# Kernel tuning notes

Measured on AMD Instinct MI355X. Metric: run time of the kernel, lower is better.

The kernel has to match this reference:

```python
import jax, jax.numpy as jnp
import numpy as np

N, E = 10000, 160000
DIN, H, DOUT, DE = 128, 256, 256, 32


def _lin(k, din, dout, scale=0.05):
    return jax.random.normal(k, (din, dout), jnp.float32) * scale


def setup_inputs() -> dict:
    key = jax.random.key(0)
    ks = jax.random.split(key, 40)
    inp = {}
    inp["x"] = jax.random.normal(ks[0], (N, DIN), jnp.float32)
    inp["edge_attr"] = jax.random.normal(ks[1], (E, DE), jnp.float32)
    inp["src"] = jax.random.randint(ks[2], (E,), 0, N, jnp.int32)
    inp["dst"] = jax.random.randint(ks[3], (E,), 0, N, jnp.int32)
    # encoders
    inp["W_edge_enc"] = _lin(ks[4], DE, H); inp["b_edge_enc"] = jnp.zeros((H,), jnp.float32)
    inp["W_node_enc"] = _lin(ks[5], DIN, H); inp["b_node_enc"] = jnp.zeros((H,), jnp.float32)
    # 3 TransformerConv layers (heads=1): q,k,v (with bias), edge (no bias), skip (with bias)
    outs = [H, H, DOUT]
    i = 6
    for l, C in enumerate(outs, start=1):
        inp[f"Wq{l}"] = _lin(ks[i], H, C); i += 1
        inp[f"bq{l}"] = jnp.zeros((C,), jnp.float32)
        inp[f"Wk{l}"] = _lin(ks[i], H, C); i += 1
        inp[f"bk{l}"] = jnp.zeros((C,), jnp.float32)
        inp[f"Wv{l}"] = _lin(ks[i], H, C); i += 1
        inp[f"bv{l}"] = jnp.zeros((C,), jnp.float32)
        inp[f"We{l}"] = _lin(ks[i], H, C); i += 1
        inp[f"Ws{l}"] = _lin(ks[i], H, C); i += 1
        inp[f"bs{l}"] = jnp.zeros((C,), jnp.float32)
    return inp


def _tconv(x, src, dst, edge_emb, Wq, bq, Wk, bk, Wv, bv, We, Ws, bs):
    # PyG TransformerConv, heads=1, concat=True, root_weight=True
    n = x.shape[0]
    C = Wq.shape[1]
    q = x @ Wq + bq            # [N, C]
    k = x @ Wk + bk            # [N, C]
    v = x @ Wv + bv            # [N, C]
    e = edge_emb @ We          # [E, C] (lin_edge, no bias)
    kj = k[src] + e            # [E, C]
    alpha = jnp.sum(q[dst] * kj, axis=-1) / jnp.sqrt(jnp.float32(C))  # [E]
    # segment softmax over incoming edges per target node
    m = jax.ops.segment_max(alpha, dst, num_segments=n)
    a = jnp.exp(alpha - m[dst])
    denom = jax.ops.segment_sum(a, dst, num_segments=n)
    a = a / jnp.maximum(denom[dst], 1e-16)
    msg = (v[src] + e) * a[:, None]                       # [E, C]
    out = jax.ops.segment_sum(msg, dst, num_segments=n)   # [N, C]
    return out + x @ Ws + bs                               # root skip


def reference(x, edge_attr, src, dst,
              W_edge_enc, b_edge_enc, W_node_enc, b_node_enc,
              Wq1, bq1, Wk1, bk1, Wv1, bv1, We1, Ws1, bs1,
              Wq2, bq2, Wk2, bk2, Wv2, bv2, We2, Ws2, bs2,
              Wq3, bq3, Wk3, bk3, Wv3, bv3, We3, Ws3, bs3):
    relu = jax.nn.relu
    edge_feat = relu(edge_attr @ W_edge_enc + b_edge_enc)  # [E, H]
    h = relu(x @ W_node_enc + b_node_enc)                  # [N, H]
    # dropout(0.3) is identity in eval mode
    h = relu(_tconv(h, src, dst, edge_feat, Wq1, bq1, Wk1, bk1, Wv1, bv1, We1, Ws1, bs1))
    h = relu(_tconv(h, src, dst, edge_feat, Wq2, bq2, Wk2, bk2, Wv2, bv2, We2, Ws2, bs2))
    h = _tconv(h, src, dst, edge_feat, Wq3, bq3, Wk3, bk3, Wv3, bv3, We3, Ws3, bs3)
    return h
```

## Files before the change

### kernel.cpp

```cpp
#include <hip/hip_runtime.h>
#include <cstdint>

typedef unsigned short u16;
typedef __attribute__((ext_vector_type(8))) short short8;
typedef __attribute__((ext_vector_type(8))) __bf16 bf16x8;
typedef __attribute__((ext_vector_type(4))) float f32x4;

#define DEV __device__ __forceinline__

DEV u16 f2bf(float f){
  uint32_t u = __float_as_uint(f);
  u += 0x7fffu + ((u >> 16) & 1u);
  return (u16)(u >> 16);
}
DEV float bf2f(u16 h){ return __uint_as_float(((uint32_t)h) << 16); }

DEV f32x4 mfma16(short8 a, short8 b, f32x4 c){
  return __builtin_amdgcn_mfma_f32_16x16x32_bf16(
      __builtin_bit_cast(bf16x8, a), __builtin_bit_cast(bf16x8, b), c, 0, 0, 0);
}

#define NN 10000
#define EE 160000
#define MPN 10112
#define MPE 160128

__global__ void count_k(const int* __restrict__ dst, int* __restrict__ cnt){
  int i = blockIdx.x * 256 + threadIdx.x;
  if(i < EE) atomicAdd(&cnt[dst[i]], 1);
}

__global__ void scan1_k(const int* __restrict__ cnt, int* __restrict__ offs,
                        int* __restrict__ bsum){
  __shared__ int buf[256];
  int b = blockIdx.x, tid = threadIdx.x, i = b * 256 + tid;
  int v = (i < NN) ? cnt[i] : 0;
  buf[tid] = v; __syncthreads();
  for(int d = 1; d < 256; d <<= 1){
    int t = (tid >= d) ? buf[tid - d] : 0;
    __syncthreads();
    buf[tid] += t;
    __syncthreads();
  }
  if(i < NN) offs[i] = buf[tid] - v;
  if(tid == 255) bsum[b] = buf[255];
}

__global__ void scan23_k(int* __restrict__ offs, const int* __restrict__ bsum,
                         int* __restrict__ cursor){
  __shared__ int bpre_s;
  int b = blockIdx.x, tid = threadIdx.x;
  if(tid == 0){
    int s = 0;
    for(int i = 0; i < b; ++i) s += bsum[i];
    bpre_s = s;
  }
  __syncthreads();
  int i = b * 256 + tid;
  if(i < NN){ int v = offs[i] + bpre_s; offs[i] = v; cursor[i] = v; }
  if(i == 0) offs[NN] = EE;
}

__global__ void scatter_k(const int* __restrict__ dst, int* __restrict__ cursor,
                          int* __restrict__ eids){
  int i = blockIdx.x * 256 + threadIdx.x;
  if(i < EE){ int p = atomicAdd(&cursor[dst[i]], 1); eids[p] = i; }
}

__global__ void rank_k(const int* __restrict__ dst, const int* __restrict__ src,
                       const int* __restrict__ offs, const int* __restrict__ eids,
                       int* __restrict__ eidp, int* __restrict__ srcp){
  int e = blockIdx.x * 256 + threadIdx.x;
  if(e >= MPE) return;
  if(e >= EE){ eidp[e] = e; return; }
  int n = dst[e];
  int p0 = offs[n], p1 = offs[n + 1];
  int rk = 0;
  for(int p = p0; p < p1; ++p) rk += (eids[p] < e) ? 1 : 0;
  int slot = p0 + rk;
  eidp[slot] = e;
  srcp[slot] = src[e];
}

struct WPack {
  const float* Wq[3]; const float* Wk[3]; const float* Wv[3];
  const float* Ws[3]; const float* We[3];
  const float* bq[3]; const float* bk[3]; const float* bv[3]; const float* bs[3];
};

#define PG0 5056
#define PG1 (PG0 + 20016)
#define PG2 (PG1 + 3840)
#define PG3 (PG2 + 1536)
#define PG4 (PG3 + 15)
#define PG5 (PG4 + 256)

__global__ __launch_bounds__(256) void prep_all_k(
    const float* __restrict__ x, const float* __restrict__ eattr, WPack P,
    const float* __restrict__ Wne, const float* __restrict__ Wee,
    u16* __restrict__ xbf, u16* __restrict__ eabf,
    u16* __restrict__ Wcat, u16* __restrict__ Wet,
    u16* __restrict__ WqBF, u16* __restrict__ WeBF,
    float* __restrict__ biasc, u16* __restrict__ Wnet, u16* __restrict__ Weet)
{
  int b = blockIdx.x, tid = threadIdx.x;
  if(b < PG0){
    int i = b * 256 + tid;
    xbf[i] = (i < NN * 128) ? f2bf(x[i]) : (u16)0;
  } else if(b < PG1){
    int i = (b - PG0) * 256 + tid;
    eabf[i] = (i < EE * 32) ? f2bf(eattr[i]) : (u16)0;
  } else if(b < PG2){
    int b2 = b - PG1; int l = b2 / 1280, r = b2 % 1280; int k = tid;
    float v;
    if(r < 256)       v = P.Wq[l][k * 256 + r];
    else if(r < 512)  v = P.Ws[l][k * 256 + (r - 256)];
    else if(r < 768){ Wet[((size_t)l * 256 + (r - 512)) * 256 + k] =
                        f2bf(P.We[l][k * 256 + (r - 512)]); return; }
    else if(r < 1024) v = P.Wk[l][k * 256 + (r - 768)];
    else              v = P.Wv[l][k * 256 + (r - 1024)];
    Wcat[((size_t)l * 1280 + r) * 256 + k] = f2bf(v);
  } else if(b < PG3){
    int b3 = b - PG2; int l = b3 >> 9, rr = b3 & 511; int t = tid;
    if(rr < 256) WqBF[((size_t)l * 256 + rr) * 256 + t] = f2bf(P.Wq[l][rr * 256 + t]);
    else         WeBF[((size_t)l * 256 + (rr - 256)) * 256 + t] = f2bf(P.We[l][(rr - 256) * 256 + t]);
  } else if(b < PG4){
    int b4 = b - PG3; int l = b4 / 5, seg = b4 % 5; int t = tid;
    float v;
    if(seg == 0)      v = P.bq[l][t];
    else if(seg == 1) v = P.bs[l][t];
    else if(seg == 2){
      const float* we = P.We[l] + (size_t)t * 256; const float* bq = P.bq[l];
      float s = 0.f;
      for(int c = 0; c < 256; ++c) s += bq[c] * we[c];
      v = s;
    }
    else if(seg == 3) v = P.bk[l][t];
    else              v = P.bv[l][t];
    biasc[(size_t)l * 1280 + seg * 256 + t] = v;
  } else {
    int n = b - PG4;
    if(tid < 128) Wnet[n * 128 + tid] = f2bf(Wne[(size_t)tid * 256 + n]);
    if(tid < 32)  Weet[n * 32 + tid]  = f2bf(Wee[(size_t)tid * 256 + n]);
  }
}

template<int BK, int EPI, int AG = 0>
__global__ __launch_bounds__(256) void gemm_k(
    const u16* __restrict__ A, const u16* __restrict__ Bt,
    const float* __restrict__ bias, void* __restrict__ Out,
    const float* __restrict__ accv, const float* __restrict__ skipS,
    const int* __restrict__ rowmap, u16* __restrict__ kvout,
    int Mreal, int Nld, int K, size_t sA, size_t sB, size_t sOb)
{
  constexpr int CPR = BK / 8;
  constexpr int SW  = (BK == 64) ? 7 : 3;
  __shared__ short8 smem8[2048];
  u16* Al = (u16*)smem8;
  u16* Bl = Al + 128 * BK;
  A  += (size_t)blockIdx.z * sA;
  Bt += (size_t)blockIdx.z * sB;
  Out = (void*)((char*)Out + (size_t)blockIdx.z * sOb);
  int tid = threadIdx.x, lane = tid & 63;
  int rowBase = blockIdx.x * 128, colBase = blockIdx.y * 128;
  int wave = tid >> 6, wm = wave >> 1, wn = wave & 1;
  int lr = lane & 15, lk = lane >> 4;
  f32x4 acc[4][4] = {};
  int nkt = K / BK;
  for(int kt = 0; kt < nkt; ++kt){
    __syncthreads();
    for(int ci = tid; ci < 128 * CPR; ci += 256){
      int r = ci / CPR, cb = ci % CPR;
      int ar = AG ? rowmap[rowBase + r] : (rowBase + r);
      int d = (r * CPR + (cb ^ (r & SW))) * 8;
      *(short8*)&Al[d] = *(const short8*)&A [(size_t)ar * K + kt * BK + cb * 8];
      *(short8*)&Bl[d] = *(const short8*)&Bt[(size_t)(colBase + r) * K + kt * BK + cb * 8];
    }
    __syncthreads();
    #pragma unroll
    for(int kk = 0; kk < BK / 32; ++kk){
      short8 af[4], bfr[4];
      #pragma unroll
      for(int m = 0; m < 4; ++m){
        int r = wm * 64 + m * 16 + lr;
        int byt = r * (BK * 2) + kk * 64 + lk * 16; byt ^= (r & SW) << 4;
        af[m] = *(const short8*)((const char*)Al + byt);
      }
      #pragma unroll
      for(int n = 0; n < 4; ++n){
        int r = wn * 64 + n * 16 + lr;
        int byt = r * (BK * 2) + kk * 64 + lk * 16; byt ^= (r & SW) << 4;
        bfr[n] = *(const short8*)((const char*)Bl + byt);
      }
      #pragma unroll
      for(int m = 0; m < 4; ++m)
        #pragma unroll
        for(int n = 0; n < 4; ++n)
          acc[m][n] = mfma16(af[m], bfr[n], acc[m][n]);
    }
  }

  __syncthreads();
  if constexpr(EPI == 0 || EPI == 4){
    bool kvside = (EPI == 0) && (colBase >= 768);
    if(kvside){
      u16* us = (u16*)smem8;
      #pragma unroll
      for(int m = 0; m < 4; ++m)
        #pragma unroll
        for(int n = 0; n < 4; ++n){
          int cc = wn * 64 + n * 16 + lr;
          #pragma unroll
          for(int j = 0; j < 4; ++j){
            int rr = wm * 64 + m * 16 + lk * 4 + j;
            us[rr * 128 + cc] = f2bf(acc[m][n][j] + bias[colBase + cc]);
          }
        }
      __syncthreads();
      for(int ch = tid; ch < 2048; ch += 256){
        int rr = ch >> 4, cc = (ch & 15) << 3;
        int r = rowBase + rr;
        if(r < Mreal)
          *(short8*)&kvout[(size_t)r * 512 + (colBase - 768) + cc] = *(short8*)&us[rr * 128 + cc];
      }
    } else {
      float* fs = (float*)smem8;
      #pragma unroll
      for(int h = 0; h < 2; ++h){
        if(wm == h){
          #pragma unroll
          for(int m = 0; m < 4; ++m)
            #pragma unroll
            for(int n = 0; n < 4; ++n){
              int cc = wn * 64 + n * 16 + lr;
              int c = colBase + cc;
              #pragma unroll
              for(int j = 0; j < 4; ++j){
                int r2 = m * 16 + lk * 4 + j;
                float v = acc[m][n][j];
                if constexpr(EPI == 0) v += bias[c];
                else {
                  int r = rowBase + h * 64 + r2;
                  v += accv[(size_t)r * 256 + c] + skipS[(size_t)r * 768 + 256 + c];
                }
                fs[r2 * 128 + cc] = v;
              }
            }
        }
        __syncthreads();
        for(int ch = tid; ch < 2048; ch += 256){
          int rr = ch >> 5, cc = (ch & 31) << 2;
          int r = rowBase + h * 64 + rr;
          if(r < Mreal)
            *(float4*)&((float*)Out)[(size_t)r * Nld + colBase + cc] = *(float4*)&fs[rr * 128 + cc];
        }
        __syncthreads();
      }
    }
  } else {
    u16* us = (u16*)smem8;
    #pragma unroll
    for(int m = 0; m < 4; ++m)
      #pragma unroll
      for(int n = 0; n < 4; ++n){
        int cc = wn * 64 + n * 16 + lr;
        int c = colBase + cc;
        #pragma unroll
        for(int j = 0; j < 4; ++j){
          int rr = wm * 64 + m * 16 + lk * 4 + j;
          float v = acc[m][n][j];
          if constexpr(EPI == 1){ v += bias[c]; v = fmaxf(v, 0.f); }
          else if constexpr(EPI == 3){
            int r = rowBase + rr;
            v += accv[(size_t)r * 256 + c] + skipS[(size_t)r * 768 + 256 + c];
            v = fmaxf(v, 0.f);
          }
          us[rr * 128 + cc] = f2bf(v);
        }
      }
    __syncthreads();
    for(int ch = tid; ch < 2048; ch += 256){
      int rr = ch >> 4, cc = (ch & 15) << 3;
      int r = rowBase + rr;
      if(r < Mreal)
        *(short8*)&((u16*)Out)[(size_t)r * Nld + colBase + cc] = *(short8*)&us[rr * 128 + cc];
    }
  }
}

__global__ __launch_bounds__(256) void node_pass_k(
    const float* __restrict__ slab, const u16* __restrict__ efp,
    const u16* __restrict__ kvbf,
    const int* __restrict__ srcp, const int* __restrict__ offs,
    float* __restrict__ accv, u16* __restrict__ aggef)
{
  int wave = threadIdx.x >> 6, lane = threadIdx.x & 63;
  int n = blockIdx.x * 4 + wave;
  if(n >= NN) return;
  int li = lane & 15, eg = lane >> 4;
  const float* qrow = slab + (size_t)n * 768 + li * 16;
  float q[16], e[16];
  #pragma unroll
  for(int t = 0; t < 4; ++t){
    float4 a = *(const float4*)(qrow + t * 4);
    float4 b = *(const float4*)(qrow + 512 + t * 4);
    q[t*4+0] = a.x; q[t*4+1] = a.y; q[t*4+2] = a.z; q[t*4+3] = a.w;
    e[t*4+0] = b.x; e[t*4+1] = b.y; e[t*4+2] = b.z; e[t*4+3] = b.w;
  }
  float av[16], ag[16];
  #pragma unroll
  for(int d = 0; d < 16; ++d){ av[d] = 0.f; ag[d] = 0.f; }
  float den = 0.f;
  int p0 = offs[n], pe = offs[n + 1];
  int p = p0 + eg;
  for(; p + 4 < pe; p += 8){
    int s1 = srcp[p], s2 = srcp[p + 4];
    const u16* kv1 = kvbf + ((size_t)s1 << 9) + li * 16;
    const u16* kv2 = kvbf + ((size_t)s2 << 9) + li * 16;
    const u16* ef1 = efp + ((size_t)p << 8) + li * 16;
    const u16* ef2 = efp + ((size_t)(p + 4) << 8) + li * 16;
    short8 kA1 = *(const short8*)(kv1),       kB1 = *(const short8*)(kv1 + 8);
    short8 vA1 = *(const short8*)(kv1 + 256), vB1 = *(const short8*)(kv1 + 264);
    short8 fA1 = *(const short8*)(ef1),       fB1 = *(const short8*)(ef1 + 8);
    short8 kA2 = *(const short8*)(kv2),       kB2 = *(const short8*)(kv2 + 8);
    short8 vA2 = *(const short8*)(kv2 + 256), vB2 = *(const short8*)(kv2 + 264);
    short8 fA2 = *(const short8*)(ef2),       fB2 = *(const short8*)(ef2 + 8);
    float sc1 = 0.f, sc2 = 0.f;
    #pragma unroll
    for(int d = 0; d < 8; ++d){
      sc1 += q[d]   * bf2f((u16)kA1[d]) + e[d]   * bf2f((u16)fA1[d]);
      sc1 += q[8+d] * bf2f((u16)kB1[d]) + e[8+d] * bf2f((u16)fB1[d]);
      sc2 += q[d]   * bf2f((u16)kA2[d]) + e[d]   * bf2f((u16)fA2[d]);
      sc2 += q[8+d] * bf2f((u16)kB2[d]) + e[8+d] * bf2f((u16)fB2[d]);
    }
    sc1 += __shfl_xor(sc1, 1); sc2 += __shfl_xor(sc2, 1);
    sc1 += __shfl_xor(sc1, 2); sc2 += __shfl_xor(sc2, 2);
    sc1 += __shfl_xor(sc1, 4); sc2 += __shfl_xor(sc2, 4);
    sc1 += __shfl_xor(sc1, 8); sc2 += __shfl_xor(sc2, 8);
    float w1 = __expf(sc1 * 0.0625f);
    float w2 = __expf(sc2 * 0.0625f);
    den += w1 + w2;
    #pragma unroll
    for(int d = 0; d < 8; ++d){
      av[d]   += w1 * bf2f((u16)vA1[d]) + w2 * bf2f((u16)vA2[d]);
      av[8+d] += w1 * bf2f((u16)vB1[d]) + w2 * bf2f((u16)vB2[d]);
      ag[d]   += w1 * bf2f((u16)fA1[d]) + w2 * bf2f((u16)fA2[d]);
      ag[8+d] += w1 * bf2f((u16)fB1[d]) + w2 * bf2f((u16)fB2[d]);
    }
  }
  if(p < pe){
    int s = srcp[p];
    const u16* kvp = kvbf + ((size_t)s << 9) + li * 16;
    const u16* epp = efp + ((size_t)p << 8) + li * 16;
    short8 kA = *(const short8*)(kvp);
    short8 kB = *(const short8*)(kvp + 8);
    short8 vA = *(const short8*)(kvp + 256);
    short8 vB = *(const short8*)(kvp + 264);
    short8 fA = *(const short8*)(epp);
    short8 fB = *(const short8*)(epp + 8);
    float part = 0.f;
    #pragma unroll
    for(int d = 0; d < 8; ++d){
      part += q[d]   * bf2f((u16)kA[d]) + e[d]   * bf2f((u16)fA[d]);
      part += q[8+d] * bf2f((u16)kB[d]) + e[8+d] * bf2f((u16)fB[d]);
    }
    part += __shfl_xor(part, 1);
    part += __shfl_xor(part, 2);
    part += __shfl_xor(part, 4);
    part += __shfl_xor(part, 8);
    float wgt = __expf(part * 0.0625f);
    den += wgt;
    #pragma unroll
    for(int d = 0; d < 8; ++d){
      av[d]   += wgt * bf2f((u16)vA[d]);
      av[8+d] += wgt * bf2f((u16)vB[d]);
      ag[d]   += wgt * bf2f((u16)fA[d]);
      ag[8+d] += wgt * bf2f((u16)fB[d]);
    }
  }
  #pragma unroll
  for(int d = 0; d < 16; ++d){
    av[d] += __shfl_xor(av[d], 16); av[d] += __shfl_xor(av[d], 32);
    ag[d] += __shfl_xor(ag[d], 16); ag[d] += __shfl_xor(ag[d], 32);
  }
  den += __shfl_xor(den, 16); den += __shfl_xor(den, 32);
  float rden = 1.f / fmaxf(den, 1e-16f);
  if(eg == 0){
    float* ao = accv + (size_t)n * 256 + li * 16;
    #pragma unroll
    for(int t = 0; t < 4; ++t){
      float4 o;
      o.x = av[t*4+0] * rden; o.y = av[t*4+1] * rden;
      o.z = av[t*4+2] * rden; o.w = av[t*4+3] * rden;
      *(float4*)(ao + t * 4) = o;
    }
  } else if(eg == 1){
    u16* go = aggef + (size_t)n * 256 + li * 16;
    #pragma unroll
    for(int t = 0; t < 2; ++t){
      short8 o;
      #pragma unroll
      for(int d = 0; d < 8; ++d) o[d] = (short)f2bf(ag[t*8+d] * rden);
      *(short8*)(go + t * 8) = o;
    }
  }
}

extern "C" void kernel_launch(void* const* d_in, const int* in_sizes, int n_in,
                              void* d_out, int out_size, void* d_ws, size_t ws_size,
                              hipStream_t stream){
  const float* x     = (const float*)d_in[0];
  const float* eattr = (const float*)d_in[1];
  const int*   src   = (const int*)d_in[2];
  const int*   dst   = (const int*)d_in[3];
  const float* Wee   = (const float*)d_in[4];
  const float* bee   = (const float*)d_in[5];
  const float* Wne   = (const float*)d_in[6];
  const float* bne   = (const float*)d_in[7];
  WPack P;
  for(int l = 0; l < 3; ++l){
    const int b = 8 + l * 9;
    P.Wq[l] = (const float*)d_in[b + 0]; P.bq[l] = (const float*)d_in[b + 1];
    P.Wk[l] = (const float*)d_in[b + 2]; P.bk[l] = (const float*)d_in[b + 3];
    P.Wv[l] = (const float*)d_in[b + 4]; P.bv[l] = (const float*)d_in[b + 5];
    P.We[l] = (const float*)d_in[b + 6];
    P.Ws[l] = (const float*)d_in[b + 7]; P.bs[l] = (const float*)d_in[b + 8];
  }

  char* w = (char*)d_ws; size_t off = 0;
  auto alloc = [&](size_t bytes)->char*{
    char* p = w + off; off = (off + bytes + 255) & ~(size_t)255; return p;
  };
  u16*   Wcat  = (u16*)  alloc((size_t)3 * 1280 * 256 * 2);
  u16*   Wet   = (u16*)  alloc((size_t)3 * 256 * 256 * 2);
  u16*   WqBF  = (u16*)  alloc((size_t)3 * 256 * 256 * 2);
  u16*   WeBF  = (u16*)  alloc((size_t)3 * 256 * 256 * 2);
  float* biasc = (float*)alloc((size_t)3 * 1280 * 4);
  u16*   Wnet  = (u16*)  alloc((size_t)256 * 128 * 2);
  u16*   Weet  = (u16*)  alloc((size_t)256 * 32 * 2);
  u16*   xbf   = (u16*)  alloc((size_t)MPN * 128 * 2);
  u16*   eabf  = (u16*)  alloc((size_t)MPE * 32 * 2);
  u16*   hbf   = (u16*)  alloc((size_t)MPN * 256 * 2);
  float* slab  = (float*)alloc((size_t)MPN * 768 * 4);
  u16*   kvbf  = (u16*)  alloc((size_t)MPN * 512 * 2);
  u16*   efp   = (u16*)  alloc((size_t)MPE * 256 * 2);
  int*   cnt   = (int*)  alloc((size_t)NN * 4);
  int*   offs  = (int*)  alloc((size_t)(NN + 1) * 4);
  int*   cursor= (int*)  alloc((size_t)NN * 4);
  int*   bsum  = (int*)  alloc((size_t)64 * 4);
  int*   eids  = (int*)  alloc((size_t)EE * 4);
  int*   eidp  = (int*)  alloc((size_t)MPE * 4);
  int*   srcp  = (int*)  alloc((size_t)EE * 4);
  float* accv  = (float*)alloc((size_t)MPN * 256 * 4);
  u16*   aggef = (u16*)  alloc((size_t)MPN * 256 * 2);
  if(off > ws_size) return;

  hipMemsetAsync(cnt, 0, (size_t)NN * 4, stream);
  count_k <<<(EE + 255) / 256, 256, 0, stream>>>(dst, cnt);
  scan1_k <<<40, 256, 0, stream>>>(cnt, offs, bsum);
  scan23_k<<<40, 256, 0, stream>>>(offs, bsum, cursor);
  scatter_k<<<(EE + 255) / 256, 256, 0, stream>>>(dst, cursor, eids);
  rank_k  <<<(MPE + 255) / 256, 256, 0, stream>>>(dst, src, offs, eids, eidp, srcp);

  prep_all_k<<<PG5, 256, 0, stream>>>(x, eattr, P, Wne, Wee,
      xbf, eabf, Wcat, Wet, WqBF, WeBF, biasc, Wnet, Weet);

  gemm_k<64,5><<<dim3(2, 2, 3), 256, 0, stream>>>(
      WeBF, WqBF, nullptr, Wcat + (size_t)512 * 256,
      nullptr, nullptr, nullptr, nullptr, 256, 256, 256,
      (size_t)256 * 256, (size_t)256 * 256, (size_t)1280 * 256 * 2);

  gemm_k<64,1><<<dim3(MPN / 128, 2), 256, 0, stream>>>(
      xbf, Wnet, bne, hbf, nullptr, nullptr, nullptr, nullptr, NN, 256, 128, 0, 0, 0);
  gemm_k<32,1,1><<<dim3(MPE / 128, 2), 256, 0, stream>>>(
      eabf, Weet, bee, efp, nullptr, nullptr, eidp, nullptr, EE, 256, 32, 0, 0, 0);

  for(int l = 0; l < 3; ++l){
    gemm_k<64,0><<<dim3(MPN / 128, 10), 256, 0, stream>>>(
        hbf, Wcat + (size_t)l * 1280 * 256, biasc + (size_t)l * 1280, slab,
        nullptr, nullptr, nullptr, kvbf, NN, 768, 256, 0, 0, 0);
    node_pass_k<<<NN / 4, 256, 0, stream>>>(slab, efp, kvbf, srcp, offs, accv, aggef);
    if(l < 2)
      gemm_k<64,3><<<dim3(MPN / 128, 2), 256, 0, stream>>>(
          aggef, Wet + (size_t)l * 256 * 256, nullptr, hbf,
          accv, slab, nullptr, nullptr, NN, 256, 256, 0, 0, 0);
    else
      gemm_k<64,4><<<dim3(MPN / 128, 2), 256, 0, stream>>>(
          aggef, Wet + (size_t)l * 256 * 256, nullptr, d_out,
          accv, slab, nullptr, nullptr, NN, 256, 256, 0, 0, 0);
  }
}
```

Baseline: 353.1 us.

## Store q/qe projections as bf16 and map one node per 16-lane group

The fused projection GEMM epilogue now writes the q and q·We sections as bf16 into a separate buffer, and the skip section as fp32 into its own compact 256-wide buffer, replacing the 768-wide fp32 slab. The node pass assigns one node to each 16-lane group instead of one per wave. Lanes load source indices cooperatively and broadcast them with shuffles, which removes the cross-group reductions. This cuts memory traffic for the slab and aims to keep lanes busy on low-degree nodes, at the cost of bf16 rounding of q and longer serial edge loops per group.

```diff
diff --git a/kernel.cpp b/kernel.cpp
--- a/kernel.cpp
+++ b/kernel.cpp
@@ -151,6 +151,7 @@
     const float* __restrict__ bias, void* __restrict__ Out,
     const float* __restrict__ accv, const float* __restrict__ skipS,
     const int* __restrict__ rowmap, u16* __restrict__ kvout,
+    float* __restrict__ skipOut,
     int Mreal, int Nld, int K, size_t sA, size_t sB, size_t sOb)
 {
   constexpr int CPR = BK / 8;
@@ -201,9 +202,35 @@
   }
 
   __syncthreads();
-  if constexpr(EPI == 0 || EPI == 4){
-    bool kvside = (EPI == 0) && (colBase >= 768);
-    if(kvside){
+  if constexpr(EPI == 0){
+    int sec = colBase >> 8;
+    if(sec == 1){
+      float* fs = (float*)smem8;
+      #pragma unroll
+      for(int h = 0; h < 2; ++h){
+        if(wm == h){
+          #pragma unroll
+          for(int m = 0; m < 4; ++m)
+            #pragma unroll
+            for(int n = 0; n < 4; ++n){
+              int cc = wn * 64 + n * 16 + lr;
+              #pragma unroll
+              for(int j = 0; j < 4; ++j){
+                int r2 = m * 16 + lk * 4 + j;
+                fs[r2 * 128 + cc] = acc[m][n][j] + bias[colBase + cc];
+              }
+            }
+        }
+        __syncthreads();
+        for(int ch = tid; ch < 2048; ch += 256){
+          int rr = ch >> 5, cc = (ch & 31) << 2;
+          int r = rowBase + h * 64 + rr;
+          if(r < Mreal)
+            *(float4*)&skipOut[(size_t)r * 256 + (colBase - 256) + cc] = *(float4*)&fs[rr * 128 + cc];
+        }
+        __syncthreads();
+      }
+    } else {
       u16* us = (u16*)smem8;
       #pragma unroll
       for(int m = 0; m < 4; ++m)
@@ -217,45 +244,45 @@
           }
         }
       __syncthreads();
+      u16* dstp; int cofs;
+      if(sec == 0){ dstp = (u16*)Out; cofs = colBase; }
+      else if(sec == 2){ dstp = (u16*)Out; cofs = colBase - 256; }
+      else { dstp = kvout; cofs = colBase - 768; }
       for(int ch = tid; ch < 2048; ch += 256){
         int rr = ch >> 4, cc = (ch & 15) << 3;
         int r = rowBase + rr;
         if(r < Mreal)
-          *(short8*)&kvout[(size_t)r * 512 + (colBase - 768) + cc] = *(short8*)&us[rr * 128 + cc];
-      }
-    } else {
-      float* fs = (float*)smem8;
-      #pragma unroll
-      for(int h = 0; h < 2; ++h){
-        if(wm == h){
+          *(short8*)&dstp[(size_t)r * 512 + cofs + cc] = *(short8*)&us[rr * 128 + cc];
+      }
+    }
+  } else if constexpr(EPI == 4){
+    float* fs = (float*)smem8;
+    #pragma unroll
+    for(int h = 0; h < 2; ++h){
+      if(wm == h){
+        #pragma unroll
+        for(int m = 0; m < 4; ++m)
           #pragma unroll
-          for(int m = 0; m < 4; ++m)
+          for(int n = 0; n < 4; ++n){
+            int cc = wn * 64 + n * 16 + lr;
+            int c = colBase + cc;
             #pragma unroll
-            for(int n = 0; n < 4; ++n){
-              int cc = wn * 64 + n * 16 + lr;
-              int c = colBase + cc;
-              #pragma unroll
-              for(int j = 0; j < 4; ++j){
-                int r2 = m * 16 + lk * 4 + j;
-                float v = acc[m][n][j];
-                if constexpr(EPI == 0) v += bias[c];
-                else {
-                  int r = rowBase + h * 64 + r2;
-                  v += accv[(size_t)r * 256 + c] + skipS[(size_t)r * 768 + 256 + c];
-                }
-                fs[r2 * 128 + cc] = v;
-              }
+            for(int j = 0; j < 4; ++j){
+              int r2 = m * 16 + lk * 4 + j;
+              int r = rowBase + h * 64 + r2;
+              fs[r2 * 128 + cc] = acc[m][n][j]
+                + accv[(size_t)r * 256 + c] + skipS[(size_t)r * 256 + c];
             }
-        }
-        __syncthreads();
-        for(int ch = tid; ch < 2048; ch += 256){
-          int rr = ch >> 5, cc = (ch & 31) << 2;
-          int r = rowBase + h * 64 + rr;
-          if(r < Mreal)
-            *(float4*)&((float*)Out)[(size_t)r * Nld + colBase + cc] = *(float4*)&fs[rr * 128 + cc];
-        }
-        __syncthreads();
-      }
+          }
+      }
+      __syncthreads();
+      for(int ch = tid; ch < 2048; ch += 256){
+        int rr = ch >> 5, cc = (ch & 31) << 2;
+        int r = rowBase + h * 64 + rr;
+        if(r < Mreal)
+          *(float4*)&((float*)Out)[(size_t)r * Nld + colBase + cc] = *(float4*)&fs[rr * 128 + cc];
+      }
+      __syncthreads();
     }
   } else {
     u16* us = (u16*)smem8;
@@ -272,7 +299,7 @@
           if constexpr(EPI == 1){ v += bias[c]; v = fmaxf(v, 0.f); }
           else if constexpr(EPI == 3){
             int r = rowBase + rr;
-            v += accv[(size_t)r * 256 + c] + skipS[(size_t)r * 768 + 256 + c];
+            v += accv[(size_t)r * 256 + c] + skipS[(size_t)r * 256 + c];
             v = fmaxf(v, 0.f);
           }
           us[rr * 128 + cc] = f2bf(v);
@@ -289,120 +316,115 @@
 }
 
 __global__ __launch_bounds__(256) void node_pass_k(
-    const float* __restrict__ slab, const u16* __restrict__ efp,
+    const u16* __restrict__ qq, const u16* __restrict__ efp,
     const u16* __restrict__ kvbf,
     const int* __restrict__ srcp, const int* __restrict__ offs,
     float* __restrict__ accv, u16* __restrict__ aggef)
 {
-  int wave = threadIdx.x >> 6, lane = threadIdx.x & 63;
-  int n = blockIdx.x * 4 + wave;
+  int tid = threadIdx.x, lane = tid & 63;
+  int li = lane & 15, gb = lane & 48;
+  int n = blockIdx.x * 16 + (tid >> 4);
   if(n >= NN) return;
-  int li = lane & 15, eg = lane >> 4;
-  const float* qrow = slab + (size_t)n * 768 + li * 16;
+  const u16* qrow = qq + (size_t)n * 512 + li * 16;
+  short8 qh0 = *(const short8*)(qrow),       qh1 = *(const short8*)(qrow + 8);
+  short8 eh0 = *(const short8*)(qrow + 256), eh1 = *(const short8*)(qrow + 264);
   float q[16], e[16];
   #pragma unroll
-  for(int t = 0; t < 4; ++t){
-    float4 a = *(const float4*)(qrow + t * 4);
-    float4 b = *(const float4*)(qrow + 512 + t * 4);
-    q[t*4+0] = a.x; q[t*4+1] = a.y; q[t*4+2] = a.z; q[t*4+3] = a.w;
-    e[t*4+0] = b.x; e[t*4+1] = b.y; e[t*4+2] = b.z; e[t*4+3] = b.w;
+  for(int d = 0; d < 8; ++d){
+    q[d] = bf2f((u16)qh0[d]); q[8 + d] = bf2f((u16)qh1[d]);
+    e[d] = bf2f((u16)eh0[d]); e[8 + d] = bf2f((u16)eh1[d]);
   }
   float av[16], ag[16];
   #pragma unroll
   for(int d = 0; d < 16; ++d){ av[d] = 0.f; ag[d] = 0.f; }
   float den = 0.f;
-  int p0 = offs[n], pe = offs[n + 1];
-  int p = p0 + eg;
-  for(; p + 4 < pe; p += 8){
-    int s1 = srcp[p], s2 = srcp[p + 4];
-    const u16* kv1 = kvbf + ((size_t)s1 << 9) + li * 16;
-    const u16* kv2 = kvbf + ((size_t)s2 << 9) + li * 16;
-    const u16* ef1 = efp + ((size_t)p << 8) + li * 16;
-    const u16* ef2 = efp + ((size_t)(p + 4) << 8) + li * 16;
-    short8 kA1 = *(const short8*)(kv1),       kB1 = *(const short8*)(kv1 + 8);
-    short8 vA1 = *(const short8*)(kv1 + 256), vB1 = *(const short8*)(kv1 + 264);
-    short8 fA1 = *(const short8*)(ef1),       fB1 = *(const short8*)(ef1 + 8);
-    short8 kA2 = *(const short8*)(kv2),       kB2 = *(const short8*)(kv2 + 8);
-    short8 vA2 = *(const short8*)(kv2 + 256), vB2 = *(const short8*)(kv2 + 264);
-    short8 fA2 = *(const short8*)(ef2),       fB2 = *(const short8*)(ef2 + 8);
-    float sc1 = 0.f, sc2 = 0.f;
+  int p0 = offs[n], deg = offs[n + 1] - p0;
+  for(int base = 0; base < deg; base += 16){
+    int scnt = deg - base; if(scnt > 16) scnt = 16;
+    int ssrc = (li < scnt) ? srcp[p0 + base + li] : 0;
+    int jj = 0;
+    for(; jj + 1 < scnt; jj += 2){
+      int s1 = __shfl(ssrc, gb + jj);
+      int s2 = __shfl(ssrc, gb + jj + 1);
+      size_t p1 = (size_t)(p0 + base + jj);
+      const u16* kv1 = kvbf + ((size_t)s1 << 9) + li * 16;
+      const u16* kv2 = kvbf + ((size_t)s2 << 9) + li * 16;
+      const u16* e1 = efp + (p1 << 8) + li * 16;
+      const u16* e2 = efp + ((p1 + 1) << 8) + li * 16;
+      short8 kA1 = *(const short8*)(kv1),       kB1 = *(const short8*)(kv1 + 8);
+      short8 vA1 = *(const short8*)(kv1 + 256), vB1 = *(const short8*)(kv1 + 264);
+      short8 fA1 = *(const short8*)(e1),        fB1 = *(const short8*)(e1 + 8);
+      short8 kA2 = *(const short8*)(kv2),       kB2 = *(const short8*)(kv2 + 8);
+      short8 vA2 = *(const short8*)(kv2 + 256), vB2 = *(const short8*)(kv2 + 264);
+      short8 fA2 = *(const short8*)(e2),        fB2 = *(const short8*)(e2 + 8);
+      float sc1 = 0.f, sc2 = 0.f;
+      #pragma unroll
+      for(int d = 0; d < 8; ++d){
+        sc1 += q[d]   * bf2f((u16)kA1[d]) + e[d]   * bf2f((u16)fA1[d]);
+        sc1 += q[8+d] * bf2f((u16)kB1[d]) + e[8+d] * bf2f((u16)fB1[d]);
+        sc2 += q[d]   * bf2f((u16)kA2[d]) + e[d]   * bf2f((u16)fA2[d]);
+        sc2 += q[8+d] * bf2f((u16)kB2[d]) + e[8+d] * bf2f((u16)fB2[d]);
+      }
+      sc1 += __shfl_xor(sc1, 1); sc2 += __shfl_xor(sc2, 1);
+      sc1 += __shfl_xor(sc1, 2); sc2 += __shfl_xor(sc2, 2);
+      sc1 += __shfl_xor(sc1, 4); sc2 += __shfl_xor(sc2, 4);
+      sc1 += __shfl_xor(sc1, 8); sc2 += __shfl_xor(sc2, 8);
+      float w1 = __expf(sc1 * 0.0625f);
+      float w2 = __expf(sc2 * 0.0625f);
+      den += w1 + w2;
+      #pragma unroll
+      for(int d = 0; d < 8; ++d){
+        av[d]   += w1 * bf2f((u16)vA1[d]) + w2 * bf2f((u16)vA2[d]);
+        av[8+d] += w1 * bf2f((u16)vB1[d]) + w2 * bf2f((u16)vB2[d]);
+        ag[d]   += w1 * bf2f((u16)fA1[d]) + w2 * bf2f((u16)fA2[d]);
+        ag[8+d] += w1 * bf2f((u16)fB1[d]) + w2 * bf2f((u16)fB2[d]);
+      }
+    }
+    if(jj < scnt){
+      int s = __shfl(ssrc, gb + jj);
+      size_t p = (size_t)(p0 + base + jj);
+      const u16* kvp = kvbf + ((size_t)s << 9) + li * 16;
+      const u16* ep = efp + (p << 8) + li * 16;
+      short8 kA = *(const short8*)(kvp),       kB = *(const short8*)(kvp + 8);
+      short8 vA = *(const short8*)(kvp + 256), vB = *(const short8*)(kvp + 264);
+      short8 fA = *(const short8*)(ep),        fB = *(const short8*)(ep + 8);
+      float part = 0.f;
+      #pragma unroll
+      for(int d = 0; d < 8; ++d){
+        part += q[d]   * bf2f((u16)kA[d]) + e[d]   * bf2f((u16)fA[d]);
+        part += q[8+d] * bf2f((u16)kB[d]) + e[8+d] * bf2f((u16)fB[d]);
+      }
+      part += __shfl_xor(part, 1);
+      part += __shfl_xor(part, 2);
+      part += __shfl_xor(part, 4);
+      part += __shfl_xor(part, 8);
+      float wgt = __expf(part * 0.0625f);
+      den += wgt;
+      #pragma unroll
+      for(int d = 0; d < 8; ++d){
+        av[d]   += wgt * bf2f((u16)vA[d]);
+        av[8+d] += wgt * bf2f((u16)vB[d]);
+        ag[d]   += wgt * bf2f((u16)fA[d]);
+        ag[8+d] += wgt * bf2f((u16)fB[d]);
+      }
+    }
+  }
+  float rden = 1.f / fmaxf(den, 1e-16f);
+  float* ao = accv + (size_t)n * 256 + li * 16;
+  #pragma unroll
+  for(int t = 0; t < 4; ++t){
+    float4 o;
+    o.x = av[t*4+0] * rden; o.y = av[t*4+1] * rden;
+    o.z = av[t*4+2] * rden; o.w = av[t*4+3] * rden;
+    *(float4*)(ao + t * 4) = o;
+  }
+  u16* go = aggef + (size_t)n * 256 + li * 16;
+  #pragma unroll
+  for(int t = 0; t < 2; ++t){
+    short8 o;
     #pragma unroll
-    for(int d = 0; d < 8; ++d){
-      sc1 += q[d]   * bf2f((u16)kA1[d]) + e[d]   * bf2f((u16)fA1[d]);
-      sc1 += q[8+d] * bf2f((u16)kB1[d]) + e[8+d] * bf2f((u16)fB1[d]);
-      sc2 += q[d]   * bf2f((u16)kA2[d]) + e[d]   * bf2f((u16)fA2[d]);
-      sc2 += q[8+d] * bf2f((u16)kB2[d]) + e[8+d] * bf2f((u16)fB2[d]);
-    }
-    sc1 += __shfl_xor(sc1, 1); sc2 += __shfl_xor(sc2, 1);
-    sc1 += __shfl_xor(sc1, 2); sc2 += __shfl_xor(sc2, 2);
-    sc1 += __shfl_xor(sc1, 4); sc2 += __shfl_xor(sc2, 4);
-    sc1 += __shfl_xor(sc1, 8); sc2 += __shfl_xor(sc2, 8);
-    float w1 = __expf(sc1 * 0.0625f);
-    float w2 = __expf(sc2 * 0.0625f);
-    den += w1 + w2;
-    #pragma unroll
-    for(int d = 0; d < 8; ++d){
-      av[d]   += w1 * bf2f((u16)vA1[d]) + w2 * bf2f((u16)vA2[d]);
-      av[8+d] += w1 * bf2f((u16)vB1[d]) + w2 * bf2f((u16)vB2[d]);
-      ag[d]   += w1 * bf2f((u16)fA1[d]) + w2 * bf2f((u16)fA2[d]);
-      ag[8+d] += w1 * bf2f((u16)fB1[d]) + w2 * bf2f((u16)fB2[d]);
-    }
-  }
-  if(p < pe){
-    int s = srcp[p];
-    const u16* kvp = kvbf + ((size_t)s << 9) + li * 16;
-    const u16* epp = efp + ((size_t)p << 8) + li * 16;
-    short8 kA = *(const short8*)(kvp);
-    short8 kB = *(const short8*)(kvp + 8);
-    short8 vA = *(const short8*)(kvp + 256);
-    short8 vB = *(const short8*)(kvp + 264);
-    short8 fA = *(const short8*)(epp);
-    short8 fB = *(const short8*)(epp + 8);
-    float part = 0.f;
-    #pragma unroll
-    for(int d = 0; d < 8; ++d){
-      part += q[d]   * bf2f((u16)kA[d]) + e[d]   * bf2f((u16)fA[d]);
-      part += q[8+d] * bf2f((u16)kB[d]) + e[8+d] * bf2f((u16)fB[d]);
-    }
-    part += __shfl_xor(part, 1);
-    part += __shfl_xor(part, 2);
-    part += __shfl_xor(part, 4);
-    part += __shfl_xor(part, 8);
-    float wgt = __expf(part * 0.0625f);
-    den += wgt;
-    #pragma unroll
-    for(int d = 0; d < 8; ++d){
-      av[d]   += wgt * bf2f((u16)vA[d]);
-      av[8+d] += wgt * bf2f((u16)vB[d]);
-      ag[d]   += wgt * bf2f((u16)fA[d]);
-      ag[8+d] += wgt * bf2f((u16)fB[d]);
-    }
-  }
-  #pragma unroll
-  for(int d = 0; d < 16; ++d){
-    av[d] += __shfl_xor(av[d], 16); av[d] += __shfl_xor(av[d], 32);
-    ag[d] += __shfl_xor(ag[d], 16); ag[d] += __shfl_xor(ag[d], 32);
-  }
-  den += __shfl_xor(den, 16); den += __shfl_xor(den, 32);
-  float rden = 1.f / fmaxf(den, 1e-16f);
-  if(eg == 0){
-    float* ao = accv + (size_t)n * 256 + li * 16;
-    #pragma unroll
-    for(int t = 0; t < 4; ++t){
-      float4 o;
-      o.x = av[t*4+0] * rden; o.y = av[t*4+1] * rden;
-      o.z = av[t*4+2] * rden; o.w = av[t*4+3] * rden;
-      *(float4*)(ao + t * 4) = o;
-    }
-  } else if(eg == 1){
-    u16* go = aggef + (size_t)n * 256 + li * 16;
-    #pragma unroll
-    for(int t = 0; t < 2; ++t){
-      short8 o;
-      #pragma unroll
-      for(int d = 0; d < 8; ++d) o[d] = (short)f2bf(ag[t*8+d] * rden);
-      *(short8*)(go + t * 8) = o;
-    }
+    for(int d = 0; d < 8; ++d) o[d] = (short)f2bf(ag[t*8+d] * rden);
+    *(short8*)(go + t * 8) = o;
   }
 }
 
@@ -441,7 +463,8 @@
   u16*   xbf   = (u16*)  alloc((size_t)MPN * 128 * 2);
   u16*   eabf  = (u16*)  alloc((size_t)MPE * 32 * 2);
   u16*   hbf   = (u16*)  alloc((size_t)MPN * 256 * 2);
-  float* slab  = (float*)alloc((size_t)MPN * 768 * 4);
+  u16*   qq    = (u16*)  alloc((size_t)MPN * 512 * 2);
+  float* skipf = (float*)alloc((size_t)MPN * 256 * 4);
   u16*   kvbf  = (u16*)  alloc((size_t)MPN * 512 * 2);
   u16*   efp   = (u16*)  alloc((size_t)MPE * 256 * 2);
   int*   cnt   = (int*)  alloc((size_t)NN * 4);
@@ -467,26 +490,28 @@
 
   gemm_k<64,5><<<dim3(2, 2, 3), 256, 0, stream>>>(
       WeBF, WqBF, nullptr, Wcat + (size_t)512 * 256,
-      nullptr, nullptr, nullptr, nullptr, 256, 256, 256,
+      nullptr, nullptr, nullptr, nullptr, nullptr, 256, 256, 256,
       (size_t)256 * 256, (size_t)256 * 256, (size_t)1280 * 256 * 2);
 
   gemm_k<64,1><<<dim3(MPN / 128, 2), 256, 0, stream>>>(
-      xbf, Wnet, bne, hbf, nullptr, nullptr, nullptr, nullptr, NN, 256, 128, 0, 0, 0);
+      xbf, Wnet, bne, hbf, nullptr, nullptr, nullptr, nullptr, nullptr,
+      NN, 256, 128, 0, 0, 0);
   gemm_k<32,1,1><<<dim3(MPE / 128, 2), 256, 0, stream>>>(
-      eabf, Weet, bee, efp, nullptr, nullptr, eidp, nullptr, EE, 256, 32, 0, 0, 0);
+      eabf, Weet, bee, efp, nullptr, nullptr, eidp, nullptr, nullptr,
+      EE, 256, 32, 0, 0, 0);
 
   for(int l = 0; l < 3; ++l){
     gemm_k<64,0><<<dim3(MPN / 128, 10), 256, 0, stream>>>(
-        hbf, Wcat + (size_t)l * 1280 * 256, biasc + (size_t)l * 1280, slab,
-        nullptr, nullptr, nullptr, kvbf, NN, 768, 256, 0, 0, 0);
-    node_pass_k<<<NN / 4, 256, 0, stream>>>(slab, efp, kvbf, srcp, offs, accv, aggef);
+        hbf, Wcat + (size_t)l * 1280 * 256, biasc + (size_t)l * 1280, qq,
+        nullptr, nullptr, nullptr, kvbf, skipf, NN, 512, 256, 0, 0, 0);
+    node_pass_k<<<625, 256, 0, stream>>>(qq, efp, kvbf, srcp, offs, accv, aggef);
     if(l < 2)
       gemm_k<64,3><<<dim3(MPN / 128, 2), 256, 0, stream>>>(
           aggef, Wet + (size_t)l * 256 * 256, nullptr, hbf,
-          accv, slab, nullptr, nullptr, NN, 256, 256, 0, 0, 0);
+          accv, skipf, nullptr, nullptr, nullptr, NN, 256, 256, 0, 0, 0);
     else
       gemm_k<64,4><<<dim3(MPN / 128, 2), 256, 0, stream>>>(
           aggef, Wet + (size_t)l * 256 * 256, nullptr, d_out,
-          accv, slab, nullptr, nullptr, NN, 256, 256, 0, 0, 0);
-  }
-}
+          accv, skipf, nullptr, nullptr, nullptr, NN, 256, 256, 0, 0, 0);
+  }
+}
```

Result: no change. 359.7 us (+1.9%).
